# Performance work log

Hardware: AMD Instinct MI355X
Metric: run time of the kernel (lower is better)

Reference implementation:

```python
import math
import jax, jax.numpy as jnp
import numpy as np

N_QUBITS = 10
N_LAYERS = 4
INPUT_DIM = 768
BATCH = 1024


def _take01(state, axis):
    s0 = jnp.take(state, jnp.array([0]), axis=axis)
    s1 = jnp.take(state, jnp.array([1]), axis=axis)
    return s0, s1


def _apply_ry(state, theta, wire):
    # state: [B] + [2]*n complex64; theta: scalar or [B]
    ax = wire + 1
    n = state.ndim - 1
    if theta.ndim == 1:
        theta = theta.reshape((-1,) + (1,) * n)
    c = jnp.cos(0.5 * theta)
    s = jnp.sin(0.5 * theta)
    s0, s1 = _take01(state, ax)
    return jnp.concatenate([c * s0 - s * s1, s * s0 + c * s1], axis=ax)


def _apply_rz(state, theta, wire):
    ax = wire + 1
    n = state.ndim - 1
    if theta.ndim == 1:
        theta = theta.reshape((-1,) + (1,) * n)
    c = jnp.cos(0.5 * theta)
    s = jnp.sin(0.5 * theta)
    e0 = (c - 1j * s).astype(jnp.complex64)  # exp(-i theta/2)
    e1 = (c + 1j * s).astype(jnp.complex64)  # exp(+i theta/2)
    s0, s1 = _take01(state, ax)
    return jnp.concatenate([e0 * s0, e1 * s1], axis=ax)


def _apply_cnot(state, ctrl, tgt):
    cax, tax = ctrl + 1, tgt + 1
    s0, s1 = _take01(state, cax)
    return jnp.concatenate([s0, jnp.flip(s1, axis=tax)], axis=cax)


def _circuit(angles, weights):
    # angles: [B, n] embedding angles; weights: [L, n, 2]
    B = angles.shape[0]
    n = N_QUBITS
    state = jnp.zeros((B,) + (2,) * n, dtype=jnp.complex64)
    state = state.at[(slice(None),) + (0,) * n].set(1.0)  # |0...0>
    # AngleEmbedding(rotation='Y')
    for w in range(n):
        state = _apply_ry(state, angles[:, w], w)
    for l in range(N_LAYERS):
        for w in range(n):
            state = _apply_ry(state, weights[l, w, 0], w)
            state = _apply_rz(state, weights[l, w, 1], w)
        for w in range(n):
            state = _apply_cnot(state, w, (w + 1) % n)
    probs = state.real ** 2 + state.imag ** 2  # [B] + [2]*n, float32
    zvals = []
    for w in range(n):
        other = tuple(a for a in range(1, n + 1) if a != w + 1)
        p = probs.sum(axis=other)  # [B, 2]
        zvals.append(p[:, 0] - p[:, 1])
    return jnp.stack(zvals, axis=-1)  # [B, n]


def setup_inputs() -> dict:
    key = jax.random.key(0)
    ks = jax.random.split(key, 6)
    x = jax.random.normal(ks[0], (BATCH, INPUT_DIM), dtype=jnp.float32)
    bound_r = 1.0 / math.sqrt(INPUT_DIM)
    Wr = jax.random.uniform(ks[1], (N_QUBITS, INPUT_DIM), jnp.float32, -bound_r, bound_r)
    br = jax.random.uniform(ks[2], (N_QUBITS,), jnp.float32, -bound_r, bound_r)
    weights = 0.01 * jax.random.normal(ks[3], (N_LAYERS, N_QUBITS, 2), dtype=jnp.float32)
    bound_o = 1.0 / math.sqrt(N_QUBITS)
    Wo = jax.random.uniform(ks[4], (1, N_QUBITS), jnp.float32, -bound_o, bound_o)
    bo = jax.random.uniform(ks[5], (1,), jnp.float32, -bound_o, bound_o)
    return {"x": x, "Wr": Wr, "br": br, "weights": weights, "Wo": Wo, "bo": bo}


def reference(x, Wr, br, weights, Wo, bo):
    reduced = jnp.tanh(x @ Wr.T + br) * (math.pi / 2.0)  # [B, n]
    expvals = _circuit(reduced, weights)                  # [B, n]
    logits = expvals @ Wo.T + bo                          # [B, 1]
    return jax.nn.sigmoid(logits[:, 0])                   # [B]
```

## Files before the change

### kernel.cpp

```cpp
#include <hip/hip_runtime.h>
#include <math.h>

#define NQ 10
#define NLAYERS 4
#define IDIM 768
#define BLK 256

constexpr int cpop(unsigned v){int c=0;for(;v;v>>=1)c+=(int)(v&1u);return c;}

struct Mats { unsigned Prow[5][NQ]; unsigned Qrow[4][NQ]; };

constexpr Mats make_mats(){
    Mats M{};
    unsigned P[NQ]={},Q[NQ]={};
    for(int b=0;b<NQ;++b){P[b]=1u<<b;Q[b]=1u<<b;}
    for(int w=0;w<NQ;++w){const int c=9-w,t=9-((w+1)%NQ);P[t]^=P[c];}
    for(int w=NQ-1;w>=0;--w){const int c=9-w,t=9-((w+1)%NQ);Q[t]^=Q[c];}
    for(int b=0;b<NQ;++b){M.Prow[0][b]=1u<<b;M.Qrow[0][b]=1u<<b;}
    for(int l=1;l<=4;++l)for(int i=0;i<NQ;++i){
        unsigned r=0;for(int j=0;j<NQ;++j)if((P[i]>>j)&1u)r^=M.Prow[l-1][j];
        M.Prow[l][i]=r;}
    for(int l=1;l<=3;++l)for(int i=0;i<NQ;++i){
        unsigned r=0;for(int j=0;j<NQ;++j)if((Q[i]>>j)&1u)r^=M.Qrow[l-1][j];
        M.Qrow[l][i]=r;}
    return M;
}
constexpr Mats MT = make_mats();

constexpr unsigned qcol(int l,int b){
    unsigned m=0;for(int j=0;j<NQ;++j)m|=((MT.Qrow[l][j]>>b)&1u)<<j;return m;
}

constexpr int BASIS[5][NQ]={
 {0,1,2,3,4,5,6,7,8,9},
 {0,1,2,3,8,5,9,7,4,6},
 {0,1,2,3,8,4,9,6,5,7},
 {0,1,5,7,8,4,9,6,2,3},
 {0,1,5,7,2,4,3,6,8,9}};

constexpr unsigned xfm(unsigned g,int bi){
    unsigned m=0;for(int p=0;p<NQ;++p)m|=((g>>BASIS[bi][p])&1u)<<p;return m;
}

constexpr int STAGE[3][NQ]={
 {1,1,0,0,0,0,0,0,0,1},
 {1,2,1,2,1,2,1,1,1,1},
 {3,3,3,4,4,2,2,2,3,2}};

constexpr int TPAIR[4][2]={{0,1},{1,2},{2,3},{3,4}};
constexpr int tsrc(int k,int p){
    const int a=TPAIR[k][0],b=TPAIR[k][1];
    const int orig=BASIS[a][p+2];
    int q=-1;for(int i=0;i<NQ;++i)if(BASIS[b][i]==orig)q=i;
    return q-2;
}

constexpr bool sched_ok(){
    for(int l=1;l<=3;++l)for(int w=0;w<NQ;++w){
        const unsigned g=qcol(l,9-w), r=MT.Prow[l][9-w];
        const int bi=STAGE[l-1][w];
        const unsigned m=xfm(g,bi), rr=xfm(r,bi);
        if(m==0) return false;
        if(m>>8) return false;
        if(!(cpop(m&rr)&1)) return false;
    }
    for(int bi=0;bi<5;++bi){
        if(BASIS[bi][0]!=0||BASIS[bi][1]!=1) return false;
        unsigned seen=0;for(int p=0;p<NQ;++p)seen|=1u<<BASIS[bi][p];
        if(seen!=0x3FFu) return false;
    }
    for(int k=0;k<4;++k)for(int p=0;p<8;++p){
        if(tsrc(k,p)<0||tsrc(k,p)>=8) return false;
    }
    return true;
}
static_assert(sched_ok(),"bad schedule");

struct RowPlan { unsigned short rt[NQ]; unsigned char rl[NQ]; };
constexpr RowPlan rplan(int l,int bi){
    RowPlan d{};
    for(int w=0;w<NQ;++w){
        const unsigned r=xfm(MT.Prow[l][9-w],bi);
        d.rt[w]=(unsigned short)(r>>2); d.rl[w]=(unsigned char)(r&3);
    }
    return d;
}
constexpr RowPlan DP1=rplan(1,1), DP2=rplan(2,2), ZP=rplan(4,4);

template<int LM>
__device__ __forceinline__ float lxor(float v){
    if constexpr (LM==0) return v;
    else if constexpr (LM<32)
        return __int_as_float(__builtin_amdgcn_ds_swizzle(__float_as_int(v),(LM<<10)|0x1F));
    else
        return __shfl_xor(v,LM,64);
}

template<int L,int W>
__device__ __forceinline__ void ry(float(&sr)[4],float(&si)[4],
                                   const float2* __restrict__ sG,int tid){
    constexpr unsigned m = xfm(qcol(L,9-W), STAGE[L-1][W]);
    constexpr unsigned r = xfm(MT.Prow[L][9-W], STAGE[L-1][W]);
    constexpr int ml=(int)(m&3u), lm=(int)((m>>2)&63u);
    constexpr int rt=(int)(r>>2), rl=(int)(r&3u);
    const float2 g = sG[(L-1)*NQ+W];
    const float cy=g.x, sy=g.y;
    const int pb=__popc(tid&rt)&1;
    const float syP = pb? sy : -sy;
    if constexpr (lm==0){
        #pragma unroll
        for(int j=0;j<4;++j){
            const int k=j^ml;
            if(j<k){
                const float sJ=((__popc(j&rl)&1)? -syP:syP);
                const float aj=sr[j],ai=si[j],bj=sr[k],bi_=si[k];
                sr[j]=fmaf(sJ,bj,cy*aj);   si[j]=fmaf(sJ,bi_,cy*ai);
                sr[k]=fmaf(-sJ,aj,cy*bj);  si[k]=fmaf(-sJ,ai,cy*bi_);
            }
        }
    } else {
        float o_r[4],o_i[4];
        #pragma unroll
        for(int q=0;q<4;++q){o_r[q]=sr[q];o_i[q]=si[q];}
        #pragma unroll
        for(int j=0;j<4;++j){
            const float pr=lxor<lm>(o_r[j^ml]);
            const float pi=lxor<lm>(o_i[j^ml]);
            const float sE=((__popc(j&rl)&1)? -syP:syP);
            sr[j]=fmaf(sE,pr,cy*o_r[j]);
            si[j]=fmaf(sE,pi,cy*o_i[j]);
        }
    }
}

template<int K>
__device__ __forceinline__ void transp(float(&sr)[4],float(&si)[4],
                                       float (*ex)[1024],int tid,int& pp){
    float* eR=ex[pp*2+0]; float* eI=ex[pp*2+1];
    const int base=tid<<2;
    *reinterpret_cast<float4*>(&eR[base])=make_float4(sr[0],sr[1],sr[2],sr[3]);
    *reinterpret_cast<float4*>(&eI[base])=make_float4(si[0],si[1],si[2],si[3]);
    __syncthreads();
    int ot=0;
    #pragma unroll
    for(int p=0;p<8;++p) ot |= ((tid>>tsrc(K,p))&1)<<p;
    const float4 qr=*reinterpret_cast<const float4*>(&eR[ot<<2]);
    const float4 qi=*reinterpret_cast<const float4*>(&eI[ot<<2]);
    sr[0]=qr.x;sr[1]=qr.y;sr[2]=qr.z;sr[3]=qr.w;
    si[0]=qi.x;si[1]=qi.y;si[2]=qi.z;si[3]=qi.w;
    pp^=1;
}

__device__ __forceinline__ void diag(float(&sr)[4],float(&si)[4],
                                     const RowPlan& dp,
                                     const float* __restrict__ hz,int tid){
    float G[4]={0.f,0.f,0.f,0.f};
    #pragma unroll
    for(int w=0;w<NQ;++w){
        const int pb=__popc(tid&dp.rt[w])&1;
        G[dp.rl[w]] += pb? hz[w] : -hz[w];
    }
    const float ph[4]={G[0]+G[1]+G[2]+G[3], G[0]-G[1]+G[2]-G[3],
                       G[0]+G[1]-G[2]-G[3], G[0]-G[1]-G[2]+G[3]};
    #pragma unroll
    for(int j=0;j<4;++j){
        float s_,c_; __sincosf(ph[j],&s_,&c_);
        const float r0=sr[j],i0=si[j];
        sr[j]=c_*r0-s_*i0;
        si[j]=c_*i0+s_*r0;
    }
}

__global__ __launch_bounds__(BLK) void qhead_kernel(
    const float* __restrict__ x,
    const float* __restrict__ Wr,
    const float* __restrict__ br,
    const float* __restrict__ wts,
    const float* __restrict__ Wo,
    const float* __restrict__ bo,
    float* __restrict__ out)
{
    __shared__ __align__(16) float sEx[4][1024];
    __shared__ __align__(8)  float2 sG2[3*NQ];
    __shared__ float sA[NQ],sCa[NQ],sSa[NQ];
    __shared__ float sHz0[NQ],sHz1[NQ],sHz2[NQ],sWo[NQ];
    __shared__ float sRed[4];
    __shared__ float sBo;

    const int t   =threadIdx.x;
    const int lane=t&63;
    const int wv  =t>>6;
    const int b   =blockIdx.x;

    if(t<60){
        const int g=t>>1,l=g/NQ+1,w=g%NQ;
        const float h=0.5f*wts[(l*NQ+w)*2];
        reinterpret_cast<float*>(sG2)[t]=(t&1)? __sinf(h):__cosf(h);
    } else if(t<70)  sHz0[t-60]=0.5f*wts[(t-60)*2+1];
    else if(t<80)    sHz1[t-70]=0.5f*wts[((t-70)+NQ)*2+1];
    else if(t<90)    sHz2[t-80]=0.5f*wts[((t-80)+2*NQ)*2+1];
    else if(t<100)   sWo[t-90]=Wo[t-90];
    else if(t==100)  sBo=bo[0];

    const float4* xp=reinterpret_cast<const float4*>(x)+(size_t)b*(IDIM/4);
    const float4 xv0=xp[lane],xv1=xp[64+lane],xv2=xp[128+lane];
    for(int q=wv;q<NQ;q+=4){
        const float4* wp=reinterpret_cast<const float4*>(Wr)+q*(IDIM/4);
        const float4 w0=wp[lane],w1=wp[64+lane],w2=wp[128+lane];
        float s=xv0.x*w0.x+xv0.y*w0.y+xv0.z*w0.z+xv0.w*w0.w
               +xv1.x*w1.x+xv1.y*w1.y+xv1.z*w1.z+xv1.w*w1.w
               +xv2.x*w2.x+xv2.y*w2.y+xv2.z*w2.z+xv2.w*w2.w;
        #pragma unroll
        for(int o=32;o;o>>=1) s+=__shfl_xor(s,o,64);
        if(lane==0){
            const float e=__expf(2.f*(s+br[q]));
            sA[q]=(1.f-__fdividef(2.f,e+1.f))*1.57079632679489662f
                 +wts[q*2];
        }
    }
    __syncthreads();

    if(t<NQ)           sCa[t]   =__cosf(0.5f*sA[t]);
    else if(t<2*NQ)    sSa[t-NQ]=__sinf(0.5f*sA[t-NQ]);
    __syncthreads();

    float ac=1.f,ph=0.f;
    #pragma unroll
    for(int w=0;w<8;++w){
        const int bit=(t>>(7-w))&1;
        ac*=bit? sSa[w]:sCa[w];
        ph+=bit? sHz0[w]:-sHz0[w];
    }
    float sr[4],si[4];
    #pragma unroll
    for(int j=0;j<4;++j){
        const float a =ac*((j&2)?sSa[8]:sCa[8])*((j&1)?sSa[9]:sCa[9]);
        const float pp_=ph+((j&2)?sHz0[8]:-sHz0[8])+((j&1)?sHz0[9]:-sHz0[9]);
        float s_,c_; __sincosf(pp_,&s_,&c_);
        sr[j]=a*c_; si[j]=a*s_;
    }

    int pp=0;
    ry<1,2>(sr,si,sG2,t); ry<1,3>(sr,si,sG2,t); ry<1,4>(sr,si,sG2,t);
    ry<1,5>(sr,si,sG2,t); ry<1,6>(sr,si,sG2,t); ry<1,7>(sr,si,sG2,t);
    ry<1,8>(sr,si,sG2,t);
    transp<0>(sr,si,sEx,t,pp);
    ry<1,0>(sr,si,sG2,t); ry<1,1>(sr,si,sG2,t); ry<1,9>(sr,si,sG2,t);
    diag(sr,si,DP1,sHz1,t);

    ry<2,0>(sr,si,sG2,t); ry<2,2>(sr,si,sG2,t); ry<2,4>(sr,si,sG2,t);
    ry<2,6>(sr,si,sG2,t); ry<2,7>(sr,si,sG2,t); ry<2,8>(sr,si,sG2,t);
    ry<2,9>(sr,si,sG2,t);
    transp<1>(sr,si,sEx,t,pp);
    ry<2,1>(sr,si,sG2,t); ry<2,3>(sr,si,sG2,t); ry<2,5>(sr,si,sG2,t);
    diag(sr,si,DP2,sHz2,t);

    ry<3,5>(sr,si,sG2,t); ry<3,6>(sr,si,sG2,t); ry<3,7>(sr,si,sG2,t);
    ry<3,9>(sr,si,sG2,t);
    transp<2>(sr,si,sEx,t,pp);
    ry<3,0>(sr,si,sG2,t); ry<3,1>(sr,si,sG2,t); ry<3,2>(sr,si,sG2,t);
    ry<3,8>(sr,si,sG2,t);
    transp<3>(sr,si,sEx,t,pp);
    ry<3,3>(sr,si,sG2,t); ry<3,4>(sr,si,sG2,t);

    float G[4]={0.f,0.f,0.f,0.f};
    #pragma unroll
    for(int w=0;w<NQ;++w){
        const int pb=__popc(t&ZP.rt[w])&1;
        G[ZP.rl[w]] += pb? -sWo[w]:sWo[w];
    }
    const float g0=G[0]+G[1]+G[2]+G[3], g1=G[0]-G[1]+G[2]-G[3];
    const float g2=G[0]+G[1]-G[2]-G[3], g3=G[0]-G[1]-G[2]+G[3];
    float acc=(sr[0]*sr[0]+si[0]*si[0])*g0;
    acc=fmaf(sr[1]*sr[1]+si[1]*si[1],g1,acc);
    acc=fmaf(sr[2]*sr[2]+si[2]*si[2],g2,acc);
    acc=fmaf(sr[3]*sr[3]+si[3]*si[3],g3,acc);
    #pragma unroll
    for(int o=32;o;o>>=1) acc+=__shfl_xor(acc,o,64);
    if(lane==0) sRed[wv]=acc;
    __syncthreads();
    if(t==0){
        const float logit=sRed[0]+sRed[1]+sRed[2]+sRed[3]+sBo;
        out[b]=__fdividef(1.f,1.f+__expf(-logit));
    }
}

extern "C" void kernel_launch(void* const* d_in, const int* in_sizes, int n_in,
                              void* d_out, int out_size, void* d_ws, size_t ws_size,
                              hipStream_t stream) {
    const float* x  =(const float*)d_in[0];
    const float* Wr =(const float*)d_in[1];
    const float* br =(const float*)d_in[2];
    const float* wts=(const float*)d_in[3];
    const float* Wo =(const float*)d_in[4];
    const float* bo =(const float*)d_in[5];
    float* out=(float*)d_out;
    const int B=in_sizes[0]/IDIM;

    qhead_kernel<<<B,BLK,0,stream>>>(x,Wr,br,wts,Wo,bo,out);
}
```

Before: 18.89 us.

## Process two batch samples per block using packed FP32 state vectors

Each block now simulates two batch elements at once. Their statevector amplitudes are held as float2 pairs and updated with v_pk_fma/v_pk_mul, which halves the block count and amortizes gate-coefficient setup, transpose syncs and reductions over two samples. The reduction stage splits the four waves into two per sample, and the shared transpose buffer and per-sample angle arrays are doubled. This trades more registers and LDS per block, and fewer blocks for the GPU to spread across CUs, for better per-instruction throughput. It also assumes the batch size is even.

```diff
diff --git a/kernel.cpp b/kernel.cpp
--- a/kernel.cpp
+++ b/kernel.cpp
@@ -5,6 +5,8 @@
 #define NLAYERS 4
 #define IDIM 768
 #define BLK 256
+
+typedef float f32x2 __attribute__((ext_vector_type(2)));
 
 constexpr int cpop(unsigned v){int c=0;for(;v;v>>=1)c+=(int)(v&1u);return c;}
 
@@ -87,6 +89,18 @@
 }
 constexpr RowPlan DP1=rplan(1,1), DP2=rplan(2,2), ZP=rplan(4,4);
 
+__device__ __forceinline__ f32x2 pk_fma(f32x2 a, f32x2 b, f32x2 c){
+    f32x2 d;
+    asm("v_pk_fma_f32 %0, %1, %2, %3" : "=v"(d) : "v"(a), "v"(b), "v"(c));
+    return d;
+}
+__device__ __forceinline__ f32x2 pk_mul(f32x2 a, f32x2 b){
+    f32x2 d;
+    asm("v_pk_mul_f32 %0, %1, %2" : "=v"(d) : "v"(a), "v"(b));
+    return d;
+}
+__device__ __forceinline__ f32x2 b2v(float s){ f32x2 r; r[0]=s; r[1]=s; return r; }
+
 template<int LM>
 __device__ __forceinline__ float lxor(float v){
     if constexpr (LM==0) return v;
@@ -95,65 +109,88 @@
     else
         return __shfl_xor(v,LM,64);
 }
+template<int LM>
+__device__ __forceinline__ f32x2 lxor2(f32x2 v){
+    f32x2 r; r[0]=lxor<LM>(v[0]); r[1]=lxor<LM>(v[1]); return r;
+}
+__device__ __forceinline__ float red64(float s){
+    s += lxor<32>(s); s += lxor<16>(s); s += lxor<8>(s);
+    s += lxor<4>(s);  s += lxor<2>(s);  s += lxor<1>(s);
+    return s;
+}
 
 template<int L,int W>
-__device__ __forceinline__ void ry(float(&sr)[4],float(&si)[4],
-                                   const float2* __restrict__ sG,int tid){
+__device__ __forceinline__ void ry2(f32x2 (&u)[4], f32x2 (&v)[4],
+                                    const float2* __restrict__ sG,int tid){
     constexpr unsigned m = xfm(qcol(L,9-W), STAGE[L-1][W]);
     constexpr unsigned r = xfm(MT.Prow[L][9-W], STAGE[L-1][W]);
     constexpr int ml=(int)(m&3u), lm=(int)((m>>2)&63u);
     constexpr int rt=(int)(r>>2), rl=(int)(r&3u);
     const float2 g = sG[(L-1)*NQ+W];
     const float cy=g.x, sy=g.y;
+    const f32x2 cy2 = b2v(cy);
     const int pb=__popc(tid&rt)&1;
     const float syP = pb? sy : -sy;
+
     if constexpr (lm==0){
         #pragma unroll
         for(int j=0;j<4;++j){
             const int k=j^ml;
             if(j<k){
                 const float sJ=((__popc(j&rl)&1)? -syP:syP);
-                const float aj=sr[j],ai=si[j],bj=sr[k],bi_=si[k];
-                sr[j]=fmaf(sJ,bj,cy*aj);   si[j]=fmaf(sJ,bi_,cy*ai);
-                sr[k]=fmaf(-sJ,aj,cy*bj);  si[k]=fmaf(-sJ,ai,cy*bi_);
+                const f32x2 sJ2=b2v(sJ), nJ2=b2v(-sJ);
+                const f32x2 aj=u[j], bk=u[k];
+                u[j]=pk_fma(bk,sJ2,pk_mul(aj,cy2));
+                u[k]=pk_fma(aj,nJ2,pk_mul(bk,cy2));
+                const f32x2 cj=v[j], dk=v[k];
+                v[j]=pk_fma(dk,sJ2,pk_mul(cj,cy2));
+                v[k]=pk_fma(cj,nJ2,pk_mul(dk,cy2));
             }
         }
     } else {
-        float o_r[4],o_i[4];
+        f32x2 ou[4],ov[4];
         #pragma unroll
-        for(int q=0;q<4;++q){o_r[q]=sr[q];o_i[q]=si[q];}
+        for(int q=0;q<4;++q){ou[q]=u[q];ov[q]=v[q];}
         #pragma unroll
         for(int j=0;j<4;++j){
-            const float pr=lxor<lm>(o_r[j^ml]);
-            const float pi=lxor<lm>(o_i[j^ml]);
+            const f32x2 pu=lxor2<lm>(ou[j^ml]);
+            const f32x2 pv=lxor2<lm>(ov[j^ml]);
             const float sE=((__popc(j&rl)&1)? -syP:syP);
-            sr[j]=fmaf(sE,pr,cy*o_r[j]);
-            si[j]=fmaf(sE,pi,cy*o_i[j]);
+            const f32x2 sE2=b2v(sE);
+            u[j]=pk_fma(pu,sE2,pk_mul(ou[j],cy2));
+            v[j]=pk_fma(pv,sE2,pk_mul(ov[j],cy2));
         }
     }
 }
 
 template<int K>
-__device__ __forceinline__ void transp(float(&sr)[4],float(&si)[4],
-                                       float (*ex)[1024],int tid,int& pp){
-    float* eR=ex[pp*2+0]; float* eI=ex[pp*2+1];
-    const int base=tid<<2;
-    *reinterpret_cast<float4*>(&eR[base])=make_float4(sr[0],sr[1],sr[2],sr[3]);
-    *reinterpret_cast<float4*>(&eI[base])=make_float4(si[0],si[1],si[2],si[3]);
+__device__ __forceinline__ void transp2(f32x2 (&u)[4], f32x2 (&v)[4],
+                                        float (*sT)[4][1024], int tid,int& pp){
+    float (*B)[1024] = sT[pp];
+    const int base = tid<<2;
+    *reinterpret_cast<float4*>(&B[0][base]) = make_float4(u[0][0],u[1][0],u[2][0],u[3][0]);
+    *reinterpret_cast<float4*>(&B[1][base]) = make_float4(u[0][1],u[1][1],u[2][1],u[3][1]);
+    *reinterpret_cast<float4*>(&B[2][base]) = make_float4(v[0][0],v[1][0],v[2][0],v[3][0]);
+    *reinterpret_cast<float4*>(&B[3][base]) = make_float4(v[0][1],v[1][1],v[2][1],v[3][1]);
     __syncthreads();
     int ot=0;
     #pragma unroll
     for(int p=0;p<8;++p) ot |= ((tid>>tsrc(K,p))&1)<<p;
-    const float4 qr=*reinterpret_cast<const float4*>(&eR[ot<<2]);
-    const float4 qi=*reinterpret_cast<const float4*>(&eI[ot<<2]);
-    sr[0]=qr.x;sr[1]=qr.y;sr[2]=qr.z;sr[3]=qr.w;
-    si[0]=qi.x;si[1]=qi.y;si[2]=qi.z;si[3]=qi.w;
+    const int ob=ot<<2;
+    const float4 r0=*reinterpret_cast<const float4*>(&B[0][ob]);
+    const float4 i0=*reinterpret_cast<const float4*>(&B[1][ob]);
+    const float4 r1=*reinterpret_cast<const float4*>(&B[2][ob]);
+    const float4 i1=*reinterpret_cast<const float4*>(&B[3][ob]);
+    u[0][0]=r0.x;u[1][0]=r0.y;u[2][0]=r0.z;u[3][0]=r0.w;
+    u[0][1]=i0.x;u[1][1]=i0.y;u[2][1]=i0.z;u[3][1]=i0.w;
+    v[0][0]=r1.x;v[1][0]=r1.y;v[2][0]=r1.z;v[3][0]=r1.w;
+    v[0][1]=i1.x;v[1][1]=i1.y;v[2][1]=i1.z;v[3][1]=i1.w;
     pp^=1;
 }
 
-__device__ __forceinline__ void diag(float(&sr)[4],float(&si)[4],
-                                     const RowPlan& dp,
-                                     const float* __restrict__ hz,int tid){
+__device__ __forceinline__ void diag2(f32x2 (&u)[4], f32x2 (&v)[4],
+                                      const RowPlan& dp,
+                                      const float* __restrict__ hz,int tid){
     float G[4]={0.f,0.f,0.f,0.f};
     #pragma unroll
     for(int w=0;w<NQ;++w){
@@ -165,9 +202,10 @@
     #pragma unroll
     for(int j=0;j<4;++j){
         float s_,c_; __sincosf(ph[j],&s_,&c_);
-        const float r0=sr[j],i0=si[j];
-        sr[j]=c_*r0-s_*i0;
-        si[j]=c_*i0+s_*r0;
+        const float xu=u[j][0], yu=u[j][1];
+        u[j][0]=fmaf(c_,xu,-s_*yu); u[j][1]=fmaf(c_,yu,s_*xu);
+        const float xv=v[j][0], yv=v[j][1];
+        v[j][0]=fmaf(c_,xv,-s_*yv); v[j][1]=fmaf(c_,yv,s_*xv);
     }
 }
 
@@ -180,17 +218,17 @@
     const float* __restrict__ bo,
     float* __restrict__ out)
 {
-    __shared__ __align__(16) float sEx[4][1024];
+    __shared__ __align__(16) float sT[2][4][1024];
     __shared__ __align__(8)  float2 sG2[3*NQ];
-    __shared__ float sA[NQ],sCa[NQ],sSa[NQ];
+    __shared__ float sA[2][NQ],sCa[2][NQ],sSa[2][NQ];
     __shared__ float sHz0[NQ],sHz1[NQ],sHz2[NQ],sWo[NQ];
-    __shared__ float sRed[4];
+    __shared__ f32x2 sRed2[4];
     __shared__ float sBo;
 
     const int t   =threadIdx.x;
     const int lane=t&63;
     const int wv  =t>>6;
-    const int b   =blockIdx.x;
+    const int bid =blockIdx.x;
 
     if(t<60){
         const int g=t>>1,l=g/NQ+1,w=g%NQ;
@@ -202,66 +240,73 @@
     else if(t<100)   sWo[t-90]=Wo[t-90];
     else if(t==100)  sBo=bo[0];
 
-    const float4* xp=reinterpret_cast<const float4*>(x)+(size_t)b*(IDIM/4);
+    const int e   = wv>>1;
+    const int qb  = wv&1;
+    const float4* xp=reinterpret_cast<const float4*>(x)
+                     +(size_t)(2*bid+e)*(IDIM/4);
     const float4 xv0=xp[lane],xv1=xp[64+lane],xv2=xp[128+lane];
-    for(int q=wv;q<NQ;q+=4){
+    #pragma unroll
+    for(int k=0;k<5;++k){
+        const int q=qb+2*k;
         const float4* wp=reinterpret_cast<const float4*>(Wr)+q*(IDIM/4);
         const float4 w0=wp[lane],w1=wp[64+lane],w2=wp[128+lane];
         float s=xv0.x*w0.x+xv0.y*w0.y+xv0.z*w0.z+xv0.w*w0.w
                +xv1.x*w1.x+xv1.y*w1.y+xv1.z*w1.z+xv1.w*w1.w
                +xv2.x*w2.x+xv2.y*w2.y+xv2.z*w2.z+xv2.w*w2.w;
-        #pragma unroll
-        for(int o=32;o;o>>=1) s+=__shfl_xor(s,o,64);
+        s=red64(s);
         if(lane==0){
-            const float e=__expf(2.f*(s+br[q]));
-            sA[q]=(1.f-__fdividef(2.f,e+1.f))*1.57079632679489662f
-                 +wts[q*2];
+            const float ex=__expf(2.f*(s+br[q]));
+            sA[e][q]=(1.f-__fdividef(2.f,ex+1.f))*1.57079632679489662f
+                    +wts[q*2];
         }
     }
     __syncthreads();
 
-    if(t<NQ)           sCa[t]   =__cosf(0.5f*sA[t]);
-    else if(t<2*NQ)    sSa[t-NQ]=__sinf(0.5f*sA[t-NQ]);
+    if(t<20)          sCa[t/NQ][t%NQ]        =__cosf(0.5f*sA[t/NQ][t%NQ]);
+    else if(t<40)     sSa[(t-20)/NQ][(t-20)%NQ]=__sinf(0.5f*sA[(t-20)/NQ][(t-20)%NQ]);
     __syncthreads();
 
-    float ac=1.f,ph=0.f;
+    float acu=1.f,acv=1.f,ph=0.f;
     #pragma unroll
     for(int w=0;w<8;++w){
         const int bit=(t>>(7-w))&1;
-        ac*=bit? sSa[w]:sCa[w];
-        ph+=bit? sHz0[w]:-sHz0[w];
-    }
-    float sr[4],si[4];
+        acu*=bit? sSa[0][w]:sCa[0][w];
+        acv*=bit? sSa[1][w]:sCa[1][w];
+        ph +=bit? sHz0[w]:-sHz0[w];
+    }
+    f32x2 u[4],v[4];
     #pragma unroll
     for(int j=0;j<4;++j){
-        const float a =ac*((j&2)?sSa[8]:sCa[8])*((j&1)?sSa[9]:sCa[9]);
+        const float aU=acu*((j&2)?sSa[0][8]:sCa[0][8])*((j&1)?sSa[0][9]:sCa[0][9]);
+        const float aV=acv*((j&2)?sSa[1][8]:sCa[1][8])*((j&1)?sSa[1][9]:sCa[1][9]);
         const float pp_=ph+((j&2)?sHz0[8]:-sHz0[8])+((j&1)?sHz0[9]:-sHz0[9]);
         float s_,c_; __sincosf(pp_,&s_,&c_);
-        sr[j]=a*c_; si[j]=a*s_;
+        u[j][0]=aU*c_; u[j][1]=aU*s_;
+        v[j][0]=aV*c_; v[j][1]=aV*s_;
     }
 
     int pp=0;
-    ry<1,2>(sr,si,sG2,t); ry<1,3>(sr,si,sG2,t); ry<1,4>(sr,si,sG2,t);
-    ry<1,5>(sr,si,sG2,t); ry<1,6>(sr,si,sG2,t); ry<1,7>(sr,si,sG2,t);
-    ry<1,8>(sr,si,sG2,t);
-    transp<0>(sr,si,sEx,t,pp);
-    ry<1,0>(sr,si,sG2,t); ry<1,1>(sr,si,sG2,t); ry<1,9>(sr,si,sG2,t);
-    diag(sr,si,DP1,sHz1,t);
-
-    ry<2,0>(sr,si,sG2,t); ry<2,2>(sr,si,sG2,t); ry<2,4>(sr,si,sG2,t);
-    ry<2,6>(sr,si,sG2,t); ry<2,7>(sr,si,sG2,t); ry<2,8>(sr,si,sG2,t);
-    ry<2,9>(sr,si,sG2,t);
-    transp<1>(sr,si,sEx,t,pp);
-    ry<2,1>(sr,si,sG2,t); ry<2,3>(sr,si,sG2,t); ry<2,5>(sr,si,sG2,t);
-    diag(sr,si,DP2,sHz2,t);
-
-    ry<3,5>(sr,si,sG2,t); ry<3,6>(sr,si,sG2,t); ry<3,7>(sr,si,sG2,t);
-    ry<3,9>(sr,si,sG2,t);
-    transp<2>(sr,si,sEx,t,pp);
-    ry<3,0>(sr,si,sG2,t); ry<3,1>(sr,si,sG2,t); ry<3,2>(sr,si,sG2,t);
-    ry<3,8>(sr,si,sG2,t);
-    transp<3>(sr,si,sEx,t,pp);
-    ry<3,3>(sr,si,sG2,t); ry<3,4>(sr,si,sG2,t);
+    ry2<1,2>(u,v,sG2,t); ry2<1,3>(u,v,sG2,t); ry2<1,4>(u,v,sG2,t);
+    ry2<1,5>(u,v,sG2,t); ry2<1,6>(u,v,sG2,t); ry2<1,7>(u,v,sG2,t);
+    ry2<1,8>(u,v,sG2,t);
+    transp2<0>(u,v,sT,t,pp);
+    ry2<1,0>(u,v,sG2,t); ry2<1,1>(u,v,sG2,t); ry2<1,9>(u,v,sG2,t);
+    diag2(u,v,DP1,sHz1,t);
+
+    ry2<2,0>(u,v,sG2,t); ry2<2,2>(u,v,sG2,t); ry2<2,4>(u,v,sG2,t);
+    ry2<2,6>(u,v,sG2,t); ry2<2,7>(u,v,sG2,t); ry2<2,8>(u,v,sG2,t);
+    ry2<2,9>(u,v,sG2,t);
+    transp2<1>(u,v,sT,t,pp);
+    ry2<2,1>(u,v,sG2,t); ry2<2,3>(u,v,sG2,t); ry2<2,5>(u,v,sG2,t);
+    diag2(u,v,DP2,sHz2,t);
+
+    ry2<3,5>(u,v,sG2,t); ry2<3,6>(u,v,sG2,t); ry2<3,7>(u,v,sG2,t);
+    ry2<3,9>(u,v,sG2,t);
+    transp2<2>(u,v,sT,t,pp);
+    ry2<3,0>(u,v,sG2,t); ry2<3,1>(u,v,sG2,t); ry2<3,2>(u,v,sG2,t);
+    ry2<3,8>(u,v,sG2,t);
+    transp2<3>(u,v,sT,t,pp);
+    ry2<3,3>(u,v,sG2,t); ry2<3,4>(u,v,sG2,t);
 
     float G[4]={0.f,0.f,0.f,0.f};
     #pragma unroll
@@ -269,19 +314,22 @@
         const int pb=__popc(t&ZP.rt[w])&1;
         G[ZP.rl[w]] += pb? -sWo[w]:sWo[w];
     }
-    const float g0=G[0]+G[1]+G[2]+G[3], g1=G[0]-G[1]+G[2]-G[3];
-    const float g2=G[0]+G[1]-G[2]-G[3], g3=G[0]-G[1]-G[2]+G[3];
-    float acc=(sr[0]*sr[0]+si[0]*si[0])*g0;
-    acc=fmaf(sr[1]*sr[1]+si[1]*si[1],g1,acc);
-    acc=fmaf(sr[2]*sr[2]+si[2]*si[2],g2,acc);
-    acc=fmaf(sr[3]*sr[3]+si[3]*si[3],g3,acc);
-    #pragma unroll
-    for(int o=32;o;o>>=1) acc+=__shfl_xor(acc,o,64);
-    if(lane==0) sRed[wv]=acc;
+    const float g[4]={G[0]+G[1]+G[2]+G[3], G[0]-G[1]+G[2]-G[3],
+                      G[0]+G[1]-G[2]-G[3], G[0]-G[1]-G[2]+G[3]};
+    f32x2 acc; acc[0]=0.f; acc[1]=0.f;
+    #pragma unroll
+    for(int j=0;j<4;++j){
+        acc[0]=fmaf(fmaf(u[j][0],u[j][0],u[j][1]*u[j][1]),g[j],acc[0]);
+        acc[1]=fmaf(fmaf(v[j][0],v[j][0],v[j][1]*v[j][1]),g[j],acc[1]);
+    }
+    acc += lxor2<32>(acc); acc += lxor2<16>(acc); acc += lxor2<8>(acc);
+    acc += lxor2<4>(acc);  acc += lxor2<2>(acc);  acc += lxor2<1>(acc);
+    if(lane==0) sRed2[wv]=acc;
     __syncthreads();
     if(t==0){
-        const float logit=sRed[0]+sRed[1]+sRed[2]+sRed[3]+sBo;
-        out[b]=__fdividef(1.f,1.f+__expf(-logit));
+        const f32x2 tot=sRed2[0]+sRed2[1]+sRed2[2]+sRed2[3];
+        out[2*bid+0]=__fdividef(1.f,1.f+__expf(-(tot[0]+sBo)));
+        out[2*bid+1]=__fdividef(1.f,1.f+__expf(-(tot[1]+sBo)));
     }
 }
 
@@ -297,5 +345,5 @@
     float* out=(float*)d_out;
     const int B=in_sizes[0]/IDIM;
 
-    qhead_kernel<<<B,BLK,0,stream>>>(x,Wr,br,wts,Wo,bo,out);
-}
+    qhead_kernel<<<B/2,BLK,0,stream>>>(x,Wr,br,wts,Wo,bo,out);
+}
```

Result: slower. 19.79 us (+4.8%).

## Pack complex amplitudes into float2 with packed FMA, DPP shuffles, new transpose bases

Applied to the files above, without the earlier changes.

Stores each complex amplitude as an interleaved float2 register pair and applies RY rotations with v_pk_fma/v_pk_mul, roughly halving VALU instruction count. Small lane-XOR exchanges now use DPP moves instead of ds_swizzle, and the wave reductions use them too. The basis permutations are redefined so transposes can move qubits into and out of the in-register bit positions, and the transpose now goes through one interleaved buffer with float2 gathers. The shared-memory footprint halves, but the gather pattern and LDS bank conflicts change and the inline asm may limit compiler scheduling.

```diff
diff --git a/kernel.cpp b/kernel.cpp
--- a/kernel.cpp
+++ b/kernel.cpp
@@ -5,6 +5,8 @@
 #define NLAYERS 4
 #define IDIM 768
 #define BLK 256
+
+typedef float f32x2 __attribute__((ext_vector_type(2)));
 
 constexpr int cpop(unsigned v){int c=0;for(;v;v>>=1)c+=(int)(v&1u);return c;}
 
@@ -33,10 +35,10 @@
 
 constexpr int BASIS[5][NQ]={
  {0,1,2,3,4,5,6,7,8,9},
- {0,1,2,3,8,5,9,7,4,6},
- {0,1,2,3,8,4,9,6,5,7},
- {0,1,5,7,8,4,9,6,2,3},
- {0,1,5,7,2,4,3,6,8,9}};
+ {8,9,7,0,1,3,5,2,4,6},
+ {4,6,2,0,8,1,3,9,5,7},
+ {6,7,8,9,5,4,0,1,2,3},
+ {3,4,5,6,2,0,1,7,8,9}};
 
 constexpr unsigned xfm(unsigned g,int bi){
     unsigned m=0;for(int p=0;p<NQ;++p)m|=((g>>BASIS[bi][p])&1u)<<p;return m;
@@ -48,11 +50,16 @@
  {3,3,3,4,4,2,2,2,3,2}};
 
 constexpr int TPAIR[4][2]={{0,1},{1,2},{2,3},{3,4}};
-constexpr int tsrc(int k,int p){
-    const int a=TPAIR[k][0],b=TPAIR[k][1];
-    const int orig=BASIS[a][p+2];
-    int q=-1;for(int i=0;i<NQ;++i)if(BASIS[b][i]==orig)q=i;
-    return q-2;
+constexpr int srcbit(int k,int p){
+    const int a=TPAIR[k][0],b2=TPAIR[k][1];
+    const int orig=BASIS[a][p];
+    int q=-1;for(int i=0;i<NQ;++i)if(BASIS[b2][i]==orig)q=i;
+    return q;
+}
+constexpr unsigned osj_tab(int k,int j){
+    unsigned os=0;
+    for(int p=0;p<NQ;++p){const int s=srcbit(k,p); if(s>=0&&s<2) os|=((unsigned)(j>>s)&1u)<<p;}
+    return os;
 }
 
 constexpr bool sched_ok(){
@@ -65,12 +72,13 @@
         if(!(cpop(m&rr)&1)) return false;
     }
     for(int bi=0;bi<5;++bi){
-        if(BASIS[bi][0]!=0||BASIS[bi][1]!=1) return false;
         unsigned seen=0;for(int p=0;p<NQ;++p)seen|=1u<<BASIS[bi][p];
         if(seen!=0x3FFu) return false;
     }
-    for(int k=0;k<4;++k)for(int p=0;p<8;++p){
-        if(tsrc(k,p)<0||tsrc(k,p)>=8) return false;
+    for(int k=0;k<4;++k){
+        unsigned seen=0;
+        for(int p=0;p<NQ;++p){const int s=srcbit(k,p); if(s<0||s>9) return false; seen|=1u<<s;}
+        if(seen!=0x3FFu) return false;
     }
     return true;
 }
@@ -87,73 +95,96 @@
 }
 constexpr RowPlan DP1=rplan(1,1), DP2=rplan(2,2), ZP=rplan(4,4);
 
+__device__ __forceinline__ f32x2 pk_fma(f32x2 a, f32x2 b, f32x2 c){
+    f32x2 d;
+    asm("v_pk_fma_f32 %0, %1, %2, %3" : "=v"(d) : "v"(a), "v"(b), "v"(c));
+    return d;
+}
+__device__ __forceinline__ f32x2 pk_mul(f32x2 a, f32x2 b){
+    f32x2 d;
+    asm("v_pk_mul_f32 %0, %1, %2" : "=v"(d) : "v"(a), "v"(b));
+    return d;
+}
+
 template<int LM>
-__device__ __forceinline__ float lxor(float v){
+__device__ __forceinline__ float lx(float v){
     if constexpr (LM==0) return v;
+    else if constexpr (LM==1)
+        return __int_as_float(__builtin_amdgcn_mov_dpp(__float_as_int(v),177,0xF,0xF,false));
+    else if constexpr (LM==2)
+        return __int_as_float(__builtin_amdgcn_mov_dpp(__float_as_int(v),78,0xF,0xF,false));
+    else if constexpr (LM==3)
+        return __int_as_float(__builtin_amdgcn_mov_dpp(__float_as_int(v),27,0xF,0xF,false));
     else if constexpr (LM<32)
         return __int_as_float(__builtin_amdgcn_ds_swizzle(__float_as_int(v),(LM<<10)|0x1F));
     else
         return __shfl_xor(v,LM,64);
 }
+__device__ __forceinline__ float red64(float s){
+    s+=lx<32>(s); s+=lx<16>(s); s+=lx<8>(s); s+=lx<4>(s); s+=lx<2>(s); s+=lx<1>(s);
+    return s;
+}
 
 template<int L,int W>
-__device__ __forceinline__ void ry(float(&sr)[4],float(&si)[4],
-                                   const float2* __restrict__ sG,int tid){
+__device__ __forceinline__ void ryp(f32x2 (&u)[4], const float2* __restrict__ sG, int tid){
     constexpr unsigned m = xfm(qcol(L,9-W), STAGE[L-1][W]);
     constexpr unsigned r = xfm(MT.Prow[L][9-W], STAGE[L-1][W]);
     constexpr int ml=(int)(m&3u), lm=(int)((m>>2)&63u);
     constexpr int rt=(int)(r>>2), rl=(int)(r&3u);
     const float2 g = sG[(L-1)*NQ+W];
-    const float cy=g.x, sy=g.y;
-    const int pb=__popc(tid&rt)&1;
-    const float syP = pb? sy : -sy;
+    const int pb = __popc(tid&rt)&1;
+    const float syP = pb ? g.y : -g.y;
+    f32x2 cy2; cy2[0]=g.x; cy2[1]=g.x;
+    f32x2 sp;  sp[0]=syP;  sp[1]=syP;
+    f32x2 sn;  sn[0]=-syP; sn[1]=-syP;
     if constexpr (lm==0){
         #pragma unroll
         for(int j=0;j<4;++j){
             const int k=j^ml;
             if(j<k){
-                const float sJ=((__popc(j&rl)&1)? -syP:syP);
-                const float aj=sr[j],ai=si[j],bj=sr[k],bi_=si[k];
-                sr[j]=fmaf(sJ,bj,cy*aj);   si[j]=fmaf(sJ,bi_,cy*ai);
-                sr[k]=fmaf(-sJ,aj,cy*bj);  si[k]=fmaf(-sJ,ai,cy*bi_);
+                const bool pj=(__popc(j&rl)&1)!=0;
+                const f32x2 sj = pj? sn:sp;
+                const f32x2 sk = pj? sp:sn;
+                const f32x2 a=u[j], b=u[k];
+                u[j]=pk_fma(b,sj,pk_mul(a,cy2));
+                u[k]=pk_fma(a,sk,pk_mul(b,cy2));
             }
         }
     } else {
-        float o_r[4],o_i[4];
-        #pragma unroll
-        for(int q=0;q<4;++q){o_r[q]=sr[q];o_i[q]=si[q];}
+        f32x2 o[4]={u[0],u[1],u[2],u[3]};
         #pragma unroll
         for(int j=0;j<4;++j){
-            const float pr=lxor<lm>(o_r[j^ml]);
-            const float pi=lxor<lm>(o_i[j^ml]);
-            const float sE=((__popc(j&rl)&1)? -syP:syP);
-            sr[j]=fmaf(sE,pr,cy*o_r[j]);
-            si[j]=fmaf(sE,pi,cy*o_i[j]);
+            f32x2 p;
+            p[0]=lx<lm>(o[j^ml][0]);
+            p[1]=lx<lm>(o[j^ml][1]);
+            const f32x2 s_=((__popc(j&rl)&1)!=0)? sn:sp;
+            u[j]=pk_fma(p,s_,pk_mul(o[j],cy2));
         }
     }
 }
 
 template<int K>
-__device__ __forceinline__ void transp(float(&sr)[4],float(&si)[4],
-                                       float (*ex)[1024],int tid,int& pp){
-    float* eR=ex[pp*2+0]; float* eI=ex[pp*2+1];
-    const int base=tid<<2;
-    *reinterpret_cast<float4*>(&eR[base])=make_float4(sr[0],sr[1],sr[2],sr[3]);
-    *reinterpret_cast<float4*>(&eI[base])=make_float4(si[0],si[1],si[2],si[3]);
+__device__ __forceinline__ void transp(f32x2 (&u)[4], f32x2* __restrict__ B, int tid){
+    float4* dst = reinterpret_cast<float4*>(&B[tid<<2]);
+    float4 d0; d0.x=u[0][0]; d0.y=u[0][1]; d0.z=u[1][0]; d0.w=u[1][1];
+    float4 d1; d1.x=u[2][0]; d1.y=u[2][1]; d1.z=u[3][0]; d1.w=u[3][1];
+    dst[0]=d0; dst[1]=d1;
     __syncthreads();
     int ot=0;
     #pragma unroll
-    for(int p=0;p<8;++p) ot |= ((tid>>tsrc(K,p))&1)<<p;
-    const float4 qr=*reinterpret_cast<const float4*>(&eR[ot<<2]);
-    const float4 qi=*reinterpret_cast<const float4*>(&eI[ot<<2]);
-    sr[0]=qr.x;sr[1]=qr.y;sr[2]=qr.z;sr[3]=qr.w;
-    si[0]=qi.x;si[1]=qi.y;si[2]=qi.z;si[3]=qi.w;
-    pp^=1;
-}
-
-__device__ __forceinline__ void diag(float(&sr)[4],float(&si)[4],
-                                     const RowPlan& dp,
-                                     const float* __restrict__ hz,int tid){
+    for(int p=0;p<NQ;++p){
+        const int s=srcbit(K,p);
+        if(s>=2) ot |= ((tid>>(s-2))&1)<<p;
+    }
+    const f32x2 r0=B[ot|osj_tab(K,0)];
+    const f32x2 r1=B[ot|osj_tab(K,1)];
+    const f32x2 r2=B[ot|osj_tab(K,2)];
+    const f32x2 r3=B[ot|osj_tab(K,3)];
+    u[0]=r0; u[1]=r1; u[2]=r2; u[3]=r3;
+}
+
+__device__ __forceinline__ void diagp(f32x2 (&u)[4], const RowPlan& dp,
+                                      const float* __restrict__ hz, int tid){
     float G[4]={0.f,0.f,0.f,0.f};
     #pragma unroll
     for(int w=0;w<NQ;++w){
@@ -165,9 +196,9 @@
     #pragma unroll
     for(int j=0;j<4;++j){
         float s_,c_; __sincosf(ph[j],&s_,&c_);
-        const float r0=sr[j],i0=si[j];
-        sr[j]=c_*r0-s_*i0;
-        si[j]=c_*i0+s_*r0;
+        const float re=u[j][0], im=u[j][1];
+        u[j][0]=fmaf(c_,re,-s_*im);
+        u[j][1]=fmaf(c_,im, s_*re);
     }
 }
 
@@ -180,7 +211,7 @@
     const float* __restrict__ bo,
     float* __restrict__ out)
 {
-    __shared__ __align__(16) float sEx[4][1024];
+    __shared__ __align__(16) f32x2 sT[2][1024];
     __shared__ __align__(8)  float2 sG2[3*NQ];
     __shared__ float sA[NQ],sCa[NQ],sSa[NQ];
     __shared__ float sHz0[NQ],sHz1[NQ],sHz2[NQ],sWo[NQ];
@@ -210,8 +241,7 @@
         float s=xv0.x*w0.x+xv0.y*w0.y+xv0.z*w0.z+xv0.w*w0.w
                +xv1.x*w1.x+xv1.y*w1.y+xv1.z*w1.z+xv1.w*w1.w
                +xv2.x*w2.x+xv2.y*w2.y+xv2.z*w2.z+xv2.w*w2.w;
-        #pragma unroll
-        for(int o=32;o;o>>=1) s+=__shfl_xor(s,o,64);
+        s=red64(s);
         if(lane==0){
             const float e=__expf(2.f*(s+br[q]));
             sA[q]=(1.f-__fdividef(2.f,e+1.f))*1.57079632679489662f
@@ -231,37 +261,37 @@
         ac*=bit? sSa[w]:sCa[w];
         ph+=bit? sHz0[w]:-sHz0[w];
     }
-    float sr[4],si[4];
+    f32x2 u[4];
     #pragma unroll
     for(int j=0;j<4;++j){
         const float a =ac*((j&2)?sSa[8]:sCa[8])*((j&1)?sSa[9]:sCa[9]);
         const float pp_=ph+((j&2)?sHz0[8]:-sHz0[8])+((j&1)?sHz0[9]:-sHz0[9]);
         float s_,c_; __sincosf(pp_,&s_,&c_);
-        sr[j]=a*c_; si[j]=a*s_;
+        u[j][0]=a*c_; u[j][1]=a*s_;
     }
 
     int pp=0;
-    ry<1,2>(sr,si,sG2,t); ry<1,3>(sr,si,sG2,t); ry<1,4>(sr,si,sG2,t);
-    ry<1,5>(sr,si,sG2,t); ry<1,6>(sr,si,sG2,t); ry<1,7>(sr,si,sG2,t);
-    ry<1,8>(sr,si,sG2,t);
-    transp<0>(sr,si,sEx,t,pp);
-    ry<1,0>(sr,si,sG2,t); ry<1,1>(sr,si,sG2,t); ry<1,9>(sr,si,sG2,t);
-    diag(sr,si,DP1,sHz1,t);
-
-    ry<2,0>(sr,si,sG2,t); ry<2,2>(sr,si,sG2,t); ry<2,4>(sr,si,sG2,t);
-    ry<2,6>(sr,si,sG2,t); ry<2,7>(sr,si,sG2,t); ry<2,8>(sr,si,sG2,t);
-    ry<2,9>(sr,si,sG2,t);
-    transp<1>(sr,si,sEx,t,pp);
-    ry<2,1>(sr,si,sG2,t); ry<2,3>(sr,si,sG2,t); ry<2,5>(sr,si,sG2,t);
-    diag(sr,si,DP2,sHz2,t);
-
-    ry<3,5>(sr,si,sG2,t); ry<3,6>(sr,si,sG2,t); ry<3,7>(sr,si,sG2,t);
-    ry<3,9>(sr,si,sG2,t);
-    transp<2>(sr,si,sEx,t,pp);
-    ry<3,0>(sr,si,sG2,t); ry<3,1>(sr,si,sG2,t); ry<3,2>(sr,si,sG2,t);
-    ry<3,8>(sr,si,sG2,t);
-    transp<3>(sr,si,sEx,t,pp);
-    ry<3,3>(sr,si,sG2,t); ry<3,4>(sr,si,sG2,t);
+    ryp<1,2>(u,sG2,t); ryp<1,3>(u,sG2,t); ryp<1,4>(u,sG2,t);
+    ryp<1,5>(u,sG2,t); ryp<1,6>(u,sG2,t); ryp<1,7>(u,sG2,t);
+    ryp<1,8>(u,sG2,t);
+    transp<0>(u,sT[pp],t); pp^=1;
+    ryp<1,0>(u,sG2,t); ryp<1,1>(u,sG2,t); ryp<1,9>(u,sG2,t);
+    diagp(u,DP1,sHz1,t);
+
+    ryp<2,0>(u,sG2,t); ryp<2,2>(u,sG2,t); ryp<2,4>(u,sG2,t);
+    ryp<2,6>(u,sG2,t); ryp<2,7>(u,sG2,t); ryp<2,8>(u,sG2,t);
+    ryp<2,9>(u,sG2,t);
+    transp<1>(u,sT[pp],t); pp^=1;
+    ryp<2,1>(u,sG2,t); ryp<2,3>(u,sG2,t); ryp<2,5>(u,sG2,t);
+    diagp(u,DP2,sHz2,t);
+
+    ryp<3,5>(u,sG2,t); ryp<3,6>(u,sG2,t); ryp<3,7>(u,sG2,t);
+    ryp<3,9>(u,sG2,t);
+    transp<2>(u,sT[pp],t); pp^=1;
+    ryp<3,0>(u,sG2,t); ryp<3,1>(u,sG2,t); ryp<3,2>(u,sG2,t);
+    ryp<3,8>(u,sG2,t);
+    transp<3>(u,sT[pp],t); pp^=1;
+    ryp<3,3>(u,sG2,t); ryp<3,4>(u,sG2,t);
 
     float G[4]={0.f,0.f,0.f,0.f};
     #pragma unroll
@@ -271,12 +301,11 @@
     }
     const float g0=G[0]+G[1]+G[2]+G[3], g1=G[0]-G[1]+G[2]-G[3];
     const float g2=G[0]+G[1]-G[2]-G[3], g3=G[0]-G[1]-G[2]+G[3];
-    float acc=(sr[0]*sr[0]+si[0]*si[0])*g0;
-    acc=fmaf(sr[1]*sr[1]+si[1]*si[1],g1,acc);
-    acc=fmaf(sr[2]*sr[2]+si[2]*si[2],g2,acc);
-    acc=fmaf(sr[3]*sr[3]+si[3]*si[3],g3,acc);
-    #pragma unroll
-    for(int o=32;o;o>>=1) acc+=__shfl_xor(acc,o,64);
+    float acc=(u[0][0]*u[0][0]+u[0][1]*u[0][1])*g0;
+    acc=fmaf(u[1][0]*u[1][0]+u[1][1]*u[1][1],g1,acc);
+    acc=fmaf(u[2][0]*u[2][0]+u[2][1]*u[2][1],g2,acc);
+    acc=fmaf(u[3][0]*u[3][0]+u[3][1]*u[3][1],g3,acc);
+    acc=red64(acc);
     if(lane==0) sRed[wv]=acc;
     __syncthreads();
     if(t==0){
```

Result: faster. 18.10 us (-4.2%).
